# Performance work log

Hardware: AMD Instinct MI355X
Metric: run time of the kernel (lower is better)

The kernel has to match this reference:

```python
import jax, jax.numpy as jnp
import numpy as np

N = 200000
E = 600000
H = 128
NUM_EDGE_TYPES = 16
LN_EPS = 1e-5


def setup_inputs() -> dict:
    key = jax.random.key(0)
    ks = jax.random.split(key, 10)
    x = jax.random.normal(ks[0], (N, H), dtype=jnp.float32)
    edge_index = jax.random.randint(ks[1], (2, E), 0, N, dtype=jnp.int32)
    edge_types = jax.random.randint(ks[2], (E,), 0, NUM_EDGE_TYPES, dtype=jnp.int32)
    s = 1.0 / np.sqrt(H)
    edge_emb = jax.random.normal(ks[3], (NUM_EDGE_TYPES, H), dtype=jnp.float32)
    W_self = jax.random.uniform(ks[4], (H, H), dtype=jnp.float32, minval=-s, maxval=s)
    b_self = jax.random.uniform(ks[5], (H,), dtype=jnp.float32, minval=-s, maxval=s)
    W_msg = jax.random.uniform(ks[6], (H, H), dtype=jnp.float32, minval=-s, maxval=s)
    b_msg = jax.random.uniform(ks[7], (H,), dtype=jnp.float32, minval=-s, maxval=s)
    gamma = jnp.ones((H,), dtype=jnp.float32)
    beta = jnp.zeros((H,), dtype=jnp.float32)
    return {
        "x": x, "edge_index": edge_index, "edge_types": edge_types,
        "edge_emb": edge_emb, "W_self": W_self, "b_self": b_self,
        "W_msg": W_msg, "b_msg": b_msg, "gamma": gamma, "beta": beta,
    }


def reference(x, edge_index, edge_types, edge_emb, W_self, b_self, W_msg, b_msg, gamma, beta):
    src = edge_index[0]
    dst = edge_index[1]
    # gather source node features + typed edge embedding: [E, H]
    typed_messages = x[src] + edge_emb[edge_types]
    # scatter-add into destination nodes: [N, H]
    aggregated = jnp.zeros_like(x).at[dst].add(typed_messages)
    # linear epilogue (torch Linear: y = x @ W.T + b)
    out = (x @ W_self.T + b_self) + (aggregated @ W_msg.T + b_msg)
    out = jax.nn.relu(out)
    # LayerNorm over last dim
    mu = jnp.mean(out, axis=-1, keepdims=True)
    var = jnp.mean(jnp.square(out - mu), axis=-1, keepdims=True)
    out = (out - mu) * jax.lax.rsqrt(var + LN_EPS) * gamma + beta
    # dropout is identity in eval mode
    return out
```

## Files before the change

kernel.cpp:

```cpp
#include <hip/hip_runtime.h>
#include <stdint.h>

#define H 128
#define TM 16
#define MAXDEG 24

typedef __attribute__((ext_vector_type(8))) short short8;
typedef __attribute__((ext_vector_type(4))) float f32x4;
typedef __attribute__((ext_vector_type(4))) int i32x4;

__device__ __forceinline__ unsigned short f2bf(float f) {
    union { float f; unsigned u; } v; v.f = f;
    unsigned u = v.u;
    u += 0x7fffu + ((u >> 16) & 1u);
    return (unsigned short)(u >> 16);
}

__device__ __forceinline__ float bf2f(unsigned short u) {
    union { unsigned u; float f; } v; v.u = ((unsigned)u) << 16; return v.f;
}

__device__ __forceinline__ short8 cvt8(f32x4 a, f32x4 b) {
    short8 r;
    r[0] = (short)f2bf(a.x); r[1] = (short)f2bf(a.y);
    r[2] = (short)f2bf(a.z); r[3] = (short)f2bf(a.w);
    r[4] = (short)f2bf(b.x); r[5] = (short)f2bf(b.y);
    r[6] = (short)f2bf(b.z); r[7] = (short)f2bf(b.w);
    return r;
}

__global__ __launch_bounds__(256) void prep_kernel(
    const float* __restrict__ x, const float* __restrict__ emb,
    unsigned short* __restrict__ xb, unsigned short* __restrict__ embb,
    const int* __restrict__ ei, const int* __restrict__ et,
    int* __restrict__ cnt, int* __restrict__ bucket,
    int total8x, int total8e, int E)
{
    int i = blockIdx.x * 256 + threadIdx.x;
    if (i < total8x) {
        f32x4 a = ((const f32x4*)x)[2 * i];
        f32x4 b = ((const f32x4*)x)[2 * i + 1];
        ((short8*)xb)[i] = cvt8(a, b);
    } else if (i < total8x + total8e) {
        int j = i - total8x;
        f32x4 a = ((const f32x4*)emb)[2 * j];
        f32x4 b = ((const f32x4*)emb)[2 * j + 1];
        ((short8*)embb)[j] = cvt8(a, b);
    }
    if (i < E) {
        int src = ei[i];
        int dst = ei[E + i];
        int t   = et[i];
        int pos = atomicAdd(&cnt[dst], 1);
        if (pos < MAXDEG) bucket[(size_t)dst * MAXDEG + pos] = src | (t << 18);
    }
}

template<bool EMB_LDS>
__global__ __launch_bounds__(256) void fused_gemm_kernel(
    const unsigned short* __restrict__ xb, const unsigned short* __restrict__ embb,
    const int* __restrict__ cnt, const int* __restrict__ bucket,
    const int* __restrict__ ei, const int* __restrict__ et,
    const float* __restrict__ Wself, const float* __restrict__ bself,
    const float* __restrict__ Wmsg, const float* __restrict__ bmsg,
    const float* __restrict__ gamma, const float* __restrict__ beta,
    float* __restrict__ out, int nTiles, int E, int T)
{
    __shared__ __align__(16) short a_stage[TM * 264];
    __shared__ __align__(16) float o_stage[TM * 132];
    __shared__ __align__(16) short emb_s[16 * 136];

    const int tid  = threadIdx.x;
    const int wave = tid >> 6;
    const int lane = tid & 63;
    const int col  = lane & 15;
    const int quad = lane >> 4;
    const int node = tid >> 4;
    const int l    = tid & 15;

    if (EMB_LDS && tid < T * 16) {
        int t = tid >> 4;
        *(short8*)&emb_s[t * 136 + l * 8] = *(const short8*)(embb + t * H + l * 8);
    }

    short8 bfrag[2][8];
    float bias[2];
#pragma unroll
    for (int s = 0; s < 2; ++s) {
        const int h = (wave * 2 + s) * 16 + col;
        bias[s] = bself[h] + bmsg[h];
#pragma unroll
        for (int kst = 0; kst < 8; ++kst) {
            const float* W = (kst < 4) ? Wself : Wmsg;
            const int k0 = (kst & 3) * 32 + quad * 8;
            const float* p = W + (size_t)h * H + k0;
            f32x4 w0 = *(const f32x4*)(p);
            f32x4 w1 = *(const f32x4*)(p + 4);
            bfrag[s][kst] = cvt8(w0, w1);
        }
    }

    const int f0 = l * 8;
    f32x4 g0  = *(const f32x4*)(gamma + f0);
    f32x4 g1  = *(const f32x4*)(gamma + f0 + 4);
    f32x4 be0 = *(const f32x4*)(beta + f0);
    f32x4 be1 = *(const f32x4*)(beta + f0 + 4);

    __syncthreads();

    for (int tile = blockIdx.x; tile < nTiles; tile += gridDim.x) {
        const size_t row = (size_t)tile * TM + node;

        short8 xv_st = *(const short8*)(xb + row * H + l * 8);

        int c = cnt[row];
        float acc[8] = {0.f, 0.f, 0.f, 0.f, 0.f, 0.f, 0.f, 0.f};
        if (c <= MAXDEG) {
            const int* b = bucket + row * MAXDEG;
            for (int i0 = 0; i0 < c; i0 += 4) {
                i32x4 p = *(const i32x4*)(b + i0);
                int rem = c - i0;
                bool h1 = rem > 1, h2 = rem > 2, h3 = rem > 3;
                short8 xv0, xv1, xv2, xv3, ev0, ev1, ev2, ev3;
                {
                    int s = p.x & 0x3FFFF, t = p.x >> 18;
                    xv0 = *(const short8*)(xb + (size_t)s * H + l * 8);
                    ev0 = EMB_LDS ? *(const short8*)&emb_s[t * 136 + l * 8]
                                  : *(const short8*)(embb + (size_t)t * H + l * 8);
                }
                if (h1) {
                    int s = p.y & 0x3FFFF, t = p.y >> 18;
                    xv1 = *(const short8*)(xb + (size_t)s * H + l * 8);
                    ev1 = EMB_LDS ? *(const short8*)&emb_s[t * 136 + l * 8]
                                  : *(const short8*)(embb + (size_t)t * H + l * 8);
                }
                if (h2) {
                    int s = p.z & 0x3FFFF, t = p.z >> 18;
                    xv2 = *(const short8*)(xb + (size_t)s * H + l * 8);
                    ev2 = EMB_LDS ? *(const short8*)&emb_s[t * 136 + l * 8]
                                  : *(const short8*)(embb + (size_t)t * H + l * 8);
                }
                if (h3) {
                    int s = p.w & 0x3FFFF, t = p.w >> 18;
                    xv3 = *(const short8*)(xb + (size_t)s * H + l * 8);
                    ev3 = EMB_LDS ? *(const short8*)&emb_s[t * 136 + l * 8]
                                  : *(const short8*)(embb + (size_t)t * H + l * 8);
                }
#pragma unroll
                for (int j = 0; j < 8; ++j) acc[j] += bf2f((unsigned short)xv0[j]) + bf2f((unsigned short)ev0[j]);
                if (h1) {
#pragma unroll
                    for (int j = 0; j < 8; ++j) acc[j] += bf2f((unsigned short)xv1[j]) + bf2f((unsigned short)ev1[j]);
                }
                if (h2) {
#pragma unroll
                    for (int j = 0; j < 8; ++j) acc[j] += bf2f((unsigned short)xv2[j]) + bf2f((unsigned short)ev2[j]);
                }
                if (h3) {
#pragma unroll
                    for (int j = 0; j < 8; ++j) acc[j] += bf2f((unsigned short)xv3[j]) + bf2f((unsigned short)ev3[j]);
                }
            }
        } else {
            for (int e = 0; e < E; ++e) {
                if (ei[E + e] == (int)row) {
                    int s = ei[e], t = et[e];
                    short8 xv = *(const short8*)(xb + (size_t)s * H + l * 8);
                    short8 ev = EMB_LDS ? *(const short8*)&emb_s[t * 136 + l * 8]
                                        : *(const short8*)(embb + (size_t)t * H + l * 8);
#pragma unroll
                    for (int j = 0; j < 8; ++j) acc[j] += bf2f((unsigned short)xv[j]) + bf2f((unsigned short)ev[j]);
                }
            }
        }

        *(short8*)&a_stage[node * 264 + l * 8] = xv_st;
        short8 ar;
#pragma unroll
        for (int j = 0; j < 8; ++j) ar[j] = (short)f2bf(acc[j]);
        *(short8*)&a_stage[node * 264 + 128 + l * 8] = ar;
        __syncthreads();

        short8 afr[8];
#pragma unroll
        for (int kst = 0; kst < 8; ++kst)
            afr[kst] = *(const short8*)(&a_stage[col * 264 + kst * 32 + quad * 8]);

        f32x4 acc0 = {0.f, 0.f, 0.f, 0.f};
        f32x4 acc1 = {0.f, 0.f, 0.f, 0.f};
#pragma unroll
        for (int kst = 0; kst < 8; ++kst) {
            acc0 = __builtin_amdgcn_mfma_f32_16x16x32_bf16(afr[kst], bfrag[0][kst], acc0, 0, 0, 0);
            acc1 = __builtin_amdgcn_mfma_f32_16x16x32_bf16(afr[kst], bfrag[1][kst], acc1, 0, 0, 0);
        }

#pragma unroll
        for (int s = 0; s < 2; ++s) {
            const int h = (wave * 2 + s) * 16 + col;
            f32x4 a = s ? acc1 : acc0;
#pragma unroll
            for (int r = 0; r < 4; ++r) {
                const int m = quad * 4 + r;
                float v = a[r] + bias[s];
                o_stage[m * 132 + h] = v > 0.f ? v : 0.f;
            }
        }
        __syncthreads();

        float v[8];
        float s1 = 0.f, s2 = 0.f;
#pragma unroll
        for (int j = 0; j < 8; ++j) {
            v[j] = o_stage[node * 132 + f0 + j];
            s1 += v[j];
            s2 += v[j] * v[j];
        }
#pragma unroll
        for (int m = 1; m < 16; m <<= 1) {
            s1 += __shfl_xor(s1, m, 64);
            s2 += __shfl_xor(s2, m, 64);
        }
        const float mu = s1 * (1.f / 128.f);
        const float var = s2 * (1.f / 128.f) - mu * mu;
        const float rstd = rsqrtf(var + 1e-5f);

        f32x4 o0, o1;
        o0.x = (v[0] - mu) * rstd * g0.x + be0.x;
        o0.y = (v[1] - mu) * rstd * g0.y + be0.y;
        o0.z = (v[2] - mu) * rstd * g0.z + be0.z;
        o0.w = (v[3] - mu) * rstd * g0.w + be0.w;
        o1.x = (v[4] - mu) * rstd * g1.x + be1.x;
        o1.y = (v[5] - mu) * rstd * g1.y + be1.y;
        o1.z = (v[6] - mu) * rstd * g1.z + be1.z;
        o1.w = (v[7] - mu) * rstd * g1.w + be1.w;

        float* dst = out + row * H + f0;
        __builtin_nontemporal_store(o0, (f32x4*)dst);
        __builtin_nontemporal_store(o1, (f32x4*)(dst + 4));
    }
}

__global__ __launch_bounds__(256) void scatter_kernel(
    const float* __restrict__ x, const int* __restrict__ ei,
    const int* __restrict__ et, const float* __restrict__ emb,
    float* __restrict__ agg, int E)
{
    int g = blockIdx.x * 256 + threadIdx.x;
    int e = g >> 5;
    int l = g & 31;
    if (e >= E) return;
    int src = ei[e];
    int dst = ei[E + e];
    int t   = et[e];
    f32x4 xv = *(const f32x4*)(x   + (size_t)src * H + l * 4);
    f32x4 ev = *(const f32x4*)(emb + (size_t)t   * H + l * 4);
    float* b = agg + (size_t)dst * H + l * 4;
    atomicAdd(b + 0, xv.x + ev.x);
    atomicAdd(b + 1, xv.y + ev.y);
    atomicAdd(b + 2, xv.z + ev.z);
    atomicAdd(b + 3, xv.w + ev.w);
}

__global__ __launch_bounds__(256) void gemm_ln_f32_kernel(
    const float* __restrict__ x,
    const float* __restrict__ Wself, const float* __restrict__ bself,
    const float* __restrict__ Wmsg, const float* __restrict__ bmsg,
    const float* __restrict__ gamma, const float* __restrict__ beta,
    float* __restrict__ out, int nTiles)
{
    __shared__ __align__(16) short a_stage[TM * 264];
    __shared__ __align__(16) float o_stage[TM * 132];

    const int tid  = threadIdx.x;
    const int wave = tid >> 6;
    const int lane = tid & 63;
    const int col  = lane & 15;
    const int quad = lane >> 4;

    short8 bfrag[2][8];
    float bias[2];
#pragma unroll
    for (int s = 0; s < 2; ++s) {
        const int h = (wave * 2 + s) * 16 + col;
        bias[s] = bself[h] + bmsg[h];
#pragma unroll
        for (int kst = 0; kst < 8; ++kst) {
            const float* W = (kst < 4) ? Wself : Wmsg;
            const int k0 = (kst & 3) * 32 + quad * 8;
            const float* p = W + (size_t)h * H + k0;
            f32x4 w0 = *(const f32x4*)(p);
            f32x4 w1 = *(const f32x4*)(p + 4);
            bfrag[s][kst] = cvt8(w0, w1);
        }
    }

    const int lnode = tid >> 4;
    const int f0 = (tid & 15) * 8;
    f32x4 g0  = *(const f32x4*)(gamma + f0);
    f32x4 g1  = *(const f32x4*)(gamma + f0 + 4);
    f32x4 be0 = *(const f32x4*)(beta + f0);
    f32x4 be1 = *(const f32x4*)(beta + f0 + 4);

    for (int tile = blockIdx.x; tile < nTiles; tile += gridDim.x) {
        const size_t rowBase = (size_t)tile * TM;
        {
            const int node = tid >> 4;
            const int seg  = tid & 15;
            const int k0   = seg * 16;
            const float* src = (seg < 8)
                ? (x   + (rowBase + node) * H + k0)
                : (out + (rowBase + node) * H + (k0 - 128));
            f32x4 v0 = ((const f32x4*)src)[0];
            f32x4 v1 = ((const f32x4*)src)[1];
            f32x4 v2 = ((const f32x4*)src)[2];
            f32x4 v3 = ((const f32x4*)src)[3];
            *(short8*)(&a_stage[node * 264 + k0])     = cvt8(v0, v1);
            *(short8*)(&a_stage[node * 264 + k0 + 8]) = cvt8(v2, v3);
        }
        __syncthreads();

        short8 afr[8];
#pragma unroll
        for (int kst = 0; kst < 8; ++kst)
            afr[kst] = *(const short8*)(&a_stage[col * 264 + kst * 32 + quad * 8]);

        f32x4 acc0 = {0.f, 0.f, 0.f, 0.f};
        f32x4 acc1 = {0.f, 0.f, 0.f, 0.f};
#pragma unroll
        for (int kst = 0; kst < 8; ++kst) {
            acc0 = __builtin_amdgcn_mfma_f32_16x16x32_bf16(afr[kst], bfrag[0][kst], acc0, 0, 0, 0);
            acc1 = __builtin_amdgcn_mfma_f32_16x16x32_bf16(afr[kst], bfrag[1][kst], acc1, 0, 0, 0);
        }

#pragma unroll
        for (int s = 0; s < 2; ++s) {
            const int h = (wave * 2 + s) * 16 + col;
            f32x4 a = s ? acc1 : acc0;
#pragma unroll
            for (int r = 0; r < 4; ++r) {
                const int m = quad * 4 + r;
                float v = a[r] + bias[s];
                o_stage[m * 132 + h] = v > 0.f ? v : 0.f;
            }
        }
        __syncthreads();

        float v[8];
        float s1 = 0.f, s2 = 0.f;
#pragma unroll
        for (int j = 0; j < 8; ++j) {
            v[j] = o_stage[lnode * 132 + f0 + j];
            s1 += v[j];
            s2 += v[j] * v[j];
        }
#pragma unroll
        for (int m = 1; m < 16; m <<= 1) {
            s1 += __shfl_xor(s1, m, 64);
            s2 += __shfl_xor(s2, m, 64);
        }
        const float mu = s1 * (1.f / 128.f);
        const float var = s2 * (1.f / 128.f) - mu * mu;
        const float rstd = rsqrtf(var + 1e-5f);

        f32x4 o0, o1;
        o0.x = (v[0] - mu) * rstd * g0.x + be0.x;
        o0.y = (v[1] - mu) * rstd * g0.y + be0.y;
        o0.z = (v[2] - mu) * rstd * g0.z + be0.z;
        o0.w = (v[3] - mu) * rstd * g0.w + be0.w;
        o1.x = (v[4] - mu) * rstd * g1.x + be1.x;
        o1.y = (v[5] - mu) * rstd * g1.y + be1.y;
        o1.z = (v[6] - mu) * rstd * g1.z + be1.z;
        o1.w = (v[7] - mu) * rstd * g1.w + be1.w;

        float* dst = out + (rowBase + lnode) * H + f0;
        *(f32x4*)(dst)     = o0;
        *(f32x4*)(dst + 4) = o1;
    }
}

extern "C" void kernel_launch(void* const* d_in, const int* in_sizes, int n_in,
                              void* d_out, int out_size, void* d_ws, size_t ws_size,
                              hipStream_t stream) {
    const float* x     = (const float*)d_in[0];
    const int*   ei    = (const int*)d_in[1];
    const int*   et    = (const int*)d_in[2];
    const float* emb   = (const float*)d_in[3];
    const float* Wself = (const float*)d_in[4];
    const float* bself = (const float*)d_in[5];
    const float* Wmsg  = (const float*)d_in[6];
    const float* bmsg  = (const float*)d_in[7];
    const float* gamma = (const float*)d_in[8];
    const float* beta  = (const float*)d_in[9];
    float* out = (float*)d_out;

    const int E = in_sizes[2];
    const int N = in_sizes[0] / H;
    const int T = in_sizes[3] / H;
    const int nTiles = N / TM;

    auto rnd = [](size_t b) { return (b + 255) & ~(size_t)255; };
    const size_t sz_xb   = rnd((size_t)N * H * 2);
    const size_t sz_embb = rnd((size_t)T * H * 2);
    const size_t sz_cnt  = rnd((size_t)N * 4);
    const size_t sz_bkt  = rnd((size_t)N * MAXDEG * 4);
    const size_t needA = sz_xb + sz_embb + sz_cnt + sz_bkt;

    const bool tierA = (ws_size >= needA) && (N <= (1 << 18)) && (T <= 4096)
                       && (N % TM == 0);

    if (tierA) {
        uint8_t* p = (uint8_t*)d_ws;
        unsigned short* xb   = (unsigned short*)p;  p += sz_xb;
        unsigned short* embb = (unsigned short*)p;  p += sz_embb;
        int* cnt    = (int*)p;                      p += sz_cnt;
        int* bucket = (int*)p;

        hipMemsetAsync(cnt, 0, (size_t)N * sizeof(int), stream);

        const int t8x = N * H / 8, t8e = T * H / 8;
        int prepWork = (t8x + t8e) > E ? (t8x + t8e) : E;
        prep_kernel<<<(prepWork + 255) / 256, 256, 0, stream>>>(
            x, emb, xb, embb, ei, et, cnt, bucket, t8x, t8e, E);

        int grid = 3125;
        if (grid > nTiles) grid = nTiles;
        if (T <= 16) {
            fused_gemm_kernel<true><<<grid, 256, 0, stream>>>(
                xb, embb, cnt, bucket, ei, et,
                Wself, bself, Wmsg, bmsg, gamma, beta, out, nTiles, E, T);
        } else {
            fused_gemm_kernel<false><<<grid, 256, 0, stream>>>(
                xb, embb, cnt, bucket, ei, et,
                Wself, bself, Wmsg, bmsg, gamma, beta, out, nTiles, E, T);
        }
    } else {
        hipMemsetAsync(out, 0, (size_t)N * H * sizeof(float), stream);
        const long long sthreads = (long long)E * 32;
        scatter_kernel<<<(int)((sthreads + 255) / 256), 256, 0, stream>>>(
            x, ei, et, emb, out, E);
        int grid = 2500;
        if (grid > nTiles) grid = nTiles;
        gemm_ln_f32_kernel<<<grid, 256, 0, stream>>>(
            x, Wself, bself, Wmsg, bmsg, gamma, beta, out, nTiles);
    }
}
```

Baseline: 334.5 us.

## Split gather-aggregate from GEMM+LN and drop bf16 copy of x

Removes the pre-pass that converted all of x and the edge embeddings to bf16. A separate aggregate kernel now gathers fp32 rows of x directly, adds the embedding from LDS, and writes a bf16 aggregate buffer. A standalone GEMM+LayerNorm kernel then converts x to bf16 on the fly and reads that buffer. This trades the x conversion pass for an extra kernel, a write and reread of the bf16 aggregate, and fp32 gathers that move twice the bytes per edge. The fast path is also limited to at most 16 edge types.

```diff
diff --git a/kernel.cpp b/kernel.cpp
--- a/kernel.cpp
+++ b/kernel.cpp
@@ -29,59 +29,118 @@
     return r;
 }
 
-__global__ __launch_bounds__(256) void prep_kernel(
+__global__ __launch_bounds__(256) void prep_edges_kernel(
+    const int* __restrict__ ei, const int* __restrict__ et,
+    int* __restrict__ cnt, int* __restrict__ bucket, int E)
+{
+    int e = blockIdx.x * 256 + threadIdx.x;
+    if (e >= E) return;
+    int src = ei[e];
+    int dst = ei[E + e];
+    int t   = et[e];
+    int pos = atomicAdd(&cnt[dst], 1);
+    if (pos < MAXDEG) bucket[(size_t)dst * MAXDEG + pos] = src | (t << 18);
+}
+
+__global__ __launch_bounds__(256) void aggregate_kernel(
     const float* __restrict__ x, const float* __restrict__ emb,
-    unsigned short* __restrict__ xb, unsigned short* __restrict__ embb,
-    const int* __restrict__ ei, const int* __restrict__ et,
-    int* __restrict__ cnt, int* __restrict__ bucket,
-    int total8x, int total8e, int E)
-{
-    int i = blockIdx.x * 256 + threadIdx.x;
-    if (i < total8x) {
-        f32x4 a = ((const f32x4*)x)[2 * i];
-        f32x4 b = ((const f32x4*)x)[2 * i + 1];
-        ((short8*)xb)[i] = cvt8(a, b);
-    } else if (i < total8x + total8e) {
-        int j = i - total8x;
-        f32x4 a = ((const f32x4*)emb)[2 * j];
-        f32x4 b = ((const f32x4*)emb)[2 * j + 1];
-        ((short8*)embb)[j] = cvt8(a, b);
-    }
-    if (i < E) {
-        int src = ei[i];
-        int dst = ei[E + i];
-        int t   = et[i];
-        int pos = atomicAdd(&cnt[dst], 1);
-        if (pos < MAXDEG) bucket[(size_t)dst * MAXDEG + pos] = src | (t << 18);
-    }
-}
-
-template<bool EMB_LDS>
-__global__ __launch_bounds__(256) void fused_gemm_kernel(
-    const unsigned short* __restrict__ xb, const unsigned short* __restrict__ embb,
     const int* __restrict__ cnt, const int* __restrict__ bucket,
     const int* __restrict__ ei, const int* __restrict__ et,
+    unsigned short* __restrict__ aggb, int N, int E, int T)
+{
+    __shared__ __align__(16) float emb_s[16 * 132];
+
+    const int tid = threadIdx.x;
+    for (int i = tid; i < T * H; i += 256)
+        emb_s[(i >> 7) * 132 + (i & 127)] = emb[i];
+    __syncthreads();
+
+    const int l = tid & 15;
+    const int nGroups = N >> 4;
+
+    for (int g = blockIdx.x; g < nGroups; g += gridDim.x) {
+        const int node = (g << 4) + (tid >> 4);
+
+        const int* b = bucket + (size_t)node * MAXDEG;
+        i32x4 p = *(const i32x4*)b;
+        const int c = cnt[node];
+
+        f32x4 acc0 = {0.f, 0.f, 0.f, 0.f};
+        f32x4 acc1 = {0.f, 0.f, 0.f, 0.f};
+
+        if (c <= MAXDEG) {
+            for (int i0 = 0; i0 < c; i0 += 4) {
+                if (i0 > 0) p = *(const i32x4*)(b + i0);
+                const int rem = c - i0;
+                const bool h1 = rem > 1, h2 = rem > 2, h3 = rem > 3;
+
+                f32x4 x00, x01, e00, e01, x10, x11, e10, e11;
+                f32x4 x20, x21, e20, e21, x30, x31, e30, e31;
+                {
+                    int s = p.x & 0x3FFFF, t = p.x >> 18;
+                    const float* xp = x + (size_t)s * H + l * 8;
+                    const float* ep = emb_s + t * 132 + l * 8;
+                    x00 = *(const f32x4*)xp;       x01 = *(const f32x4*)(xp + 4);
+                    e00 = *(const f32x4*)ep;       e01 = *(const f32x4*)(ep + 4);
+                }
+                if (h1) {
+                    int s = p.y & 0x3FFFF, t = p.y >> 18;
+                    const float* xp = x + (size_t)s * H + l * 8;
+                    const float* ep = emb_s + t * 132 + l * 8;
+                    x10 = *(const f32x4*)xp;       x11 = *(const f32x4*)(xp + 4);
+                    e10 = *(const f32x4*)ep;       e11 = *(const f32x4*)(ep + 4);
+                }
+                if (h2) {
+                    int s = p.z & 0x3FFFF, t = p.z >> 18;
+                    const float* xp = x + (size_t)s * H + l * 8;
+                    const float* ep = emb_s + t * 132 + l * 8;
+                    x20 = *(const f32x4*)xp;       x21 = *(const f32x4*)(xp + 4);
+                    e20 = *(const f32x4*)ep;       e21 = *(const f32x4*)(ep + 4);
+                }
+                if (h3) {
+                    int s = p.w & 0x3FFFF, t = p.w >> 18;
+                    const float* xp = x + (size_t)s * H + l * 8;
+                    const float* ep = emb_s + t * 132 + l * 8;
+                    x30 = *(const f32x4*)xp;       x31 = *(const f32x4*)(xp + 4);
+                    e30 = *(const f32x4*)ep;       e31 = *(const f32x4*)(ep + 4);
+                }
+                acc0 += x00 + e00;  acc1 += x01 + e01;
+                if (h1) { acc0 += x10 + e10;  acc1 += x11 + e11; }
+                if (h2) { acc0 += x20 + e20;  acc1 += x21 + e21; }
+                if (h3) { acc0 += x30 + e30;  acc1 += x31 + e31; }
+            }
+        } else {
+            for (int e = 0; e < E; ++e) {
+                if (ei[E + e] == node) {
+                    int s = ei[e], t = et[e];
+                    const float* xp = x + (size_t)s * H + l * 8;
+                    const float* ep = emb_s + t * 132 + l * 8;
+                    f32x4 v0 = *(const f32x4*)xp, v1 = *(const f32x4*)(xp + 4);
+                    f32x4 w0 = *(const f32x4*)ep, w1 = *(const f32x4*)(ep + 4);
+                    acc0 += v0 + w0;  acc1 += v1 + w1;
+                }
+            }
+        }
+
+        *(short8*)(aggb + (size_t)node * H + l * 8) = cvt8(acc0, acc1);
+    }
+}
+
+__global__ __launch_bounds__(256) void gemm_ln_kernel(
+    const float* __restrict__ x, const unsigned short* __restrict__ aggb,
     const float* __restrict__ Wself, const float* __restrict__ bself,
     const float* __restrict__ Wmsg, const float* __restrict__ bmsg,
     const float* __restrict__ gamma, const float* __restrict__ beta,
-    float* __restrict__ out, int nTiles, int E, int T)
+    float* __restrict__ out, int nTiles)
 {
     __shared__ __align__(16) short a_stage[TM * 264];
     __shared__ __align__(16) float o_stage[TM * 132];
-    __shared__ __align__(16) short emb_s[16 * 136];
 
     const int tid  = threadIdx.x;
     const int wave = tid >> 6;
     const int lane = tid & 63;
     const int col  = lane & 15;
     const int quad = lane >> 4;
-    const int node = tid >> 4;
-    const int l    = tid & 15;
-
-    if (EMB_LDS && tid < T * 16) {
-        int t = tid >> 4;
-        *(short8*)&emb_s[t * 136 + l * 8] = *(const short8*)(embb + t * H + l * 8);
-    }
 
     short8 bfrag[2][8];
     float bias[2];
@@ -100,85 +159,32 @@
         }
     }
 
-    const int f0 = l * 8;
+    const int lnode = tid >> 4;
+    const int f0 = (tid & 15) * 8;
     f32x4 g0  = *(const f32x4*)(gamma + f0);
     f32x4 g1  = *(const f32x4*)(gamma + f0 + 4);
     f32x4 be0 = *(const f32x4*)(beta + f0);
     f32x4 be1 = *(const f32x4*)(beta + f0 + 4);
 
-    __syncthreads();
+    const int node = tid >> 4;
+    const int seg  = tid & 15;
 
     for (int tile = blockIdx.x; tile < nTiles; tile += gridDim.x) {
-        const size_t row = (size_t)tile * TM + node;
-
-        short8 xv_st = *(const short8*)(xb + row * H + l * 8);
-
-        int c = cnt[row];
-        float acc[8] = {0.f, 0.f, 0.f, 0.f, 0.f, 0.f, 0.f, 0.f};
-        if (c <= MAXDEG) {
-            const int* b = bucket + row * MAXDEG;
-            for (int i0 = 0; i0 < c; i0 += 4) {
-                i32x4 p = *(const i32x4*)(b + i0);
-                int rem = c - i0;
-                bool h1 = rem > 1, h2 = rem > 2, h3 = rem > 3;
-                short8 xv0, xv1, xv2, xv3, ev0, ev1, ev2, ev3;
-                {
-                    int s = p.x & 0x3FFFF, t = p.x >> 18;
-                    xv0 = *(const short8*)(xb + (size_t)s * H + l * 8);
-                    ev0 = EMB_LDS ? *(const short8*)&emb_s[t * 136 + l * 8]
-                                  : *(const short8*)(embb + (size_t)t * H + l * 8);
-                }
-                if (h1) {
-                    int s = p.y & 0x3FFFF, t = p.y >> 18;
-                    xv1 = *(const short8*)(xb + (size_t)s * H + l * 8);
-                    ev1 = EMB_LDS ? *(const short8*)&emb_s[t * 136 + l * 8]
-                                  : *(const short8*)(embb + (size_t)t * H + l * 8);
-                }
-                if (h2) {
-                    int s = p.z & 0x3FFFF, t = p.z >> 18;
-                    xv2 = *(const short8*)(xb + (size_t)s * H + l * 8);
-                    ev2 = EMB_LDS ? *(const short8*)&emb_s[t * 136 + l * 8]
-                                  : *(const short8*)(embb + (size_t)t * H + l * 8);
-                }
-                if (h3) {
-                    int s = p.w & 0x3FFFF, t = p.w >> 18;
-                    xv3 = *(const short8*)(xb + (size_t)s * H + l * 8);
-                    ev3 = EMB_LDS ? *(const short8*)&emb_s[t * 136 + l * 8]
-                                  : *(const short8*)(embb + (size_t)t * H + l * 8);
-                }
-#pragma unroll
-                for (int j = 0; j < 8; ++j) acc[j] += bf2f((unsigned short)xv0[j]) + bf2f((unsigned short)ev0[j]);
-                if (h1) {
-#pragma unroll
-                    for (int j = 0; j < 8; ++j) acc[j] += bf2f((unsigned short)xv1[j]) + bf2f((unsigned short)ev1[j]);
-                }
-                if (h2) {
-#pragma unroll
-                    for (int j = 0; j < 8; ++j) acc[j] += bf2f((unsigned short)xv2[j]) + bf2f((unsigned short)ev2[j]);
-                }
-                if (h3) {
-#pragma unroll
-                    for (int j = 0; j < 8; ++j) acc[j] += bf2f((unsigned short)xv3[j]) + bf2f((unsigned short)ev3[j]);
-                }
-            }
+        const size_t rowBase = (size_t)tile * TM;
+
+        if (seg < 8) {
+            const float* src = x + (rowBase + node) * H + seg * 16;
+            f32x4 v0 = ((const f32x4*)src)[0];
+            f32x4 v1 = ((const f32x4*)src)[1];
+            f32x4 v2 = ((const f32x4*)src)[2];
+            f32x4 v3 = ((const f32x4*)src)[3];
+            *(short8*)&a_stage[node * 264 + seg * 16]     = cvt8(v0, v1);
+            *(short8*)&a_stage[node * 264 + seg * 16 + 8] = cvt8(v2, v3);
         } else {
-            for (int e = 0; e < E; ++e) {
-                if (ei[E + e] == (int)row) {
-                    int s = ei[e], t = et[e];
-                    short8 xv = *(const short8*)(xb + (size_t)s * H + l * 8);
-                    short8 ev = EMB_LDS ? *(const short8*)&emb_s[t * 136 + l * 8]
-                                        : *(const short8*)(embb + (size_t)t * H + l * 8);
-#pragma unroll
-                    for (int j = 0; j < 8; ++j) acc[j] += bf2f((unsigned short)xv[j]) + bf2f((unsigned short)ev[j]);
-                }
-            }
-        }
-
-        *(short8*)&a_stage[node * 264 + l * 8] = xv_st;
-        short8 ar;
-#pragma unroll
-        for (int j = 0; j < 8; ++j) ar[j] = (short)f2bf(acc[j]);
-        *(short8*)&a_stage[node * 264 + 128 + l * 8] = ar;
+            const unsigned short* src = aggb + (rowBase + node) * H + (seg - 8) * 16;
+            *(short8*)&a_stage[node * 264 + 128 + (seg - 8) * 16]     = *(const short8*)src;
+            *(short8*)&a_stage[node * 264 + 128 + (seg - 8) * 16 + 8] = *(const short8*)(src + 8);
+        }
         __syncthreads();
 
         short8 afr[8];
@@ -211,7 +217,7 @@
         float s1 = 0.f, s2 = 0.f;
 #pragma unroll
         for (int j = 0; j < 8; ++j) {
-            v[j] = o_stage[node * 132 + f0 + j];
+            v[j] = o_stage[lnode * 132 + f0 + j];
             s1 += v[j];
             s2 += v[j] * v[j];
         }
@@ -234,7 +240,7 @@
         o1.z = (v[6] - mu) * rstd * g1.z + be1.z;
         o1.w = (v[7] - mu) * rstd * g1.w + be1.w;
 
-        float* dst = out + row * H + f0;
+        float* dst = out + (rowBase + lnode) * H + f0;
         __builtin_nontemporal_store(o0, (f32x4*)dst);
         __builtin_nontemporal_store(o1, (f32x4*)(dst + 4));
     }
@@ -399,40 +405,35 @@
     const int nTiles = N / TM;
 
     auto rnd = [](size_t b) { return (b + 255) & ~(size_t)255; };
-    const size_t sz_xb   = rnd((size_t)N * H * 2);
-    const size_t sz_embb = rnd((size_t)T * H * 2);
-    const size_t sz_cnt  = rnd((size_t)N * 4);
-    const size_t sz_bkt  = rnd((size_t)N * MAXDEG * 4);
-    const size_t needA = sz_xb + sz_embb + sz_cnt + sz_bkt;
-
-    const bool tierA = (ws_size >= needA) && (N <= (1 << 18)) && (T <= 4096)
+    const size_t sz_agg = rnd((size_t)N * H * 2);
+    const size_t sz_cnt = rnd((size_t)N * 4);
+    const size_t sz_bkt = rnd((size_t)N * MAXDEG * 4);
+    const size_t needA = sz_agg + sz_cnt + sz_bkt;
+
+    const bool tierA = (ws_size >= needA) && (N <= (1 << 18)) && (T <= 16)
                        && (N % TM == 0);
 
     if (tierA) {
         uint8_t* p = (uint8_t*)d_ws;
-        unsigned short* xb   = (unsigned short*)p;  p += sz_xb;
-        unsigned short* embb = (unsigned short*)p;  p += sz_embb;
+        unsigned short* aggb = (unsigned short*)p;  p += sz_agg;
         int* cnt    = (int*)p;                      p += sz_cnt;
         int* bucket = (int*)p;
 
         hipMemsetAsync(cnt, 0, (size_t)N * sizeof(int), stream);
 
-        const int t8x = N * H / 8, t8e = T * H / 8;
-        int prepWork = (t8x + t8e) > E ? (t8x + t8e) : E;
-        prep_kernel<<<(prepWork + 255) / 256, 256, 0, stream>>>(
-            x, emb, xb, embb, ei, et, cnt, bucket, t8x, t8e, E);
-
-        int grid = 3125;
-        if (grid > nTiles) grid = nTiles;
-        if (T <= 16) {
-            fused_gemm_kernel<true><<<grid, 256, 0, stream>>>(
-                xb, embb, cnt, bucket, ei, et,
-                Wself, bself, Wmsg, bmsg, gamma, beta, out, nTiles, E, T);
-        } else {
-            fused_gemm_kernel<false><<<grid, 256, 0, stream>>>(
-                xb, embb, cnt, bucket, ei, et,
-                Wself, bself, Wmsg, bmsg, gamma, beta, out, nTiles, E, T);
-        }
+        if (E > 0) {
+            prep_edges_kernel<<<(E + 255) / 256, 256, 0, stream>>>(
+                ei, et, cnt, bucket, E);
+        }
+
+        const int nGroups = N >> 4;
+        int aggGrid = nGroups < 4096 ? nGroups : 4096;
+        aggregate_kernel<<<aggGrid, 256, 0, stream>>>(
+            x, emb, cnt, bucket, ei, et, aggb, N, E, T);
+
+        int gemmGrid = nTiles < 2048 ? nTiles : 2048;
+        gemm_ln_kernel<<<gemmGrid, 256, 0, stream>>>(
+            x, aggb, Wself, bself, Wmsg, bmsg, gamma, beta, out, nTiles);
     } else {
         hipMemsetAsync(out, 0, (size_t)N * H * sizeof(float), stream);
         const long long sthreads = (long long)E * 32;
```

After: 338.4 us. No clear change (+1.1%).
